# Kernel tuning notes

Hardware: AMD Instinct MI355X
Metric: run time of the kernel (lower is better)

## Reference

```python
import jax, jax.numpy as jnp
import numpy as np
import math

B, S, H = 2, 2048, 2048
NH, HD = 32, 64
BASE, SCALE = 10000.0, 2.0
MAX_POS, ORIG_MAX_POS = 8192, 8192
BETA_FAST, BETA_SLOW = 32, 1
EPS = 1e-6


def _yarn_cos_sin():
    # revised_yarn: scale inv_freq by 1/((1-mask)*scale + mask)
    inv_freq = 1.0 / BASE ** (np.arange(0, HD, 2, dtype=np.float64) / HD)
    def corr(nr):
        return HD * math.log(ORIG_MAX_POS / (nr * 2 * math.pi)) / (2 * math.log(BASE))
    low = max(math.floor(corr(BETA_FAST)), 0)
    high = min(math.ceil(corr(BETA_SLOW)), HD - 1)
    hi = high + 0.001 if low == high else high
    ramp = np.clip((np.arange(HD // 2, dtype=np.float64) - low) / (hi - low), 0.0, 1.0)
    mask = 1.0 - ramp  # extrapolation_factor = 1
    inv_freq = inv_freq / ((1.0 - mask) * SCALE + mask)
    mscale = (0.1 * math.log(SCALE) + 1.0) if SCALE > 1 else 1.0
    t = np.arange(MAX_POS, dtype=np.float64)
    freqs = np.outer(t, inv_freq)
    emb = np.concatenate([freqs, freqs], axis=-1)
    return np.cos(emb) * mscale, np.sin(emb) * mscale

_COS_NP, _SIN_NP = _yarn_cos_sin()


def rotate_half(x):
    x1, x2 = jnp.split(x, 2, axis=-1)
    return jnp.concatenate([-x2, x1], axis=-1)


def rms_norm(x, w):
    v = jnp.mean(jnp.square(x.astype(jnp.float32)), axis=-1, keepdims=True)
    return (x.astype(jnp.float32) * jax.lax.rsqrt(v + EPS)).astype(x.dtype) * w


def localized_filtering(x, lf1, lf2, w1, b1, w2, b2, ln_w):
    # x: (B,S,H); torch works in (B,H,S,1) with kernel-(2,1) convs over seq
    residual = x
    xi = jnp.transpose(x, (0, 2, 1))[:, :, :, None]  # (B,H,S,1)
    xi = jnp.concatenate([lf1, xi], axis=2)          # (B,H,S+1,1)
    dn = ('NCHW', 'OIHW', 'NCHW')
    o1 = jax.lax.conv_general_dilated(xi, w1, (1, 1), 'VALID', dimension_numbers=dn)
    o1 = o1 + b1[None, :, None, None]                # (B,H/2,S,1)
    o1c = jnp.concatenate([lf2, o1], axis=2)         # (B,H/2,S+1,1)
    o2 = jax.lax.conv_general_dilated(o1c, w2, (1, 1), 'VALID', dimension_numbers=dn)
    o2 = o2 + b2[None, :, None, None]                # (B,H,S,1)
    o2 = jnp.transpose(o2[:, :, :, 0], (0, 2, 1))    # (B,S,H)
    return rms_norm(o2 + residual, ln_w)


def setup_inputs():
    key = jax.random.key(0)
    ks = jax.random.split(key, 8)
    f = lambda k, shp: jax.random.normal(k, shp, dtype=jnp.float32) * 0.02
    return {
        'hidden_states': jax.random.normal(ks[0], (B, S, H), dtype=jnp.float32),
        'position_ids': jnp.broadcast_to(jnp.arange(S, dtype=jnp.int32)[None, :], (B, S)),
        'lf1_cache': jnp.zeros((B, H, 1, 1), jnp.float32),
        'lf2_cache': jnp.zeros((B, H // 2, 1, 1), jnp.float32),
        'Wqk': f(ks[1], (2 * H, H)),
        'Wv': f(ks[2], (H, H)),
        'Wo': f(ks[3], (H, H)),
        'conv1_w': f(ks[4], (H // 2, H, 2, 1)),
        'conv1_b': jnp.zeros((H // 2,), jnp.float32),
        'conv2_w': f(ks[5], (H, H // 2, 2, 1)),
        'conv2_b': jnp.zeros((H,), jnp.float32),
        'ln_w': jnp.ones((H,), jnp.float32),
    }


def reference(hidden_states, position_ids, lf1_cache, lf2_cache, Wqk, Wv, Wo,
              conv1_w, conv1_b, conv2_w, conv2_b, ln_w):
    cos = jnp.asarray(_COS_NP, jnp.float32)
    sin = jnp.asarray(_SIN_NP, jnp.float32)
    # v from raw hidden states
    v = (hidden_states @ Wv.T).reshape(B, S, NH, HD).transpose(0, 2, 1, 3)  # (B,NH,S,HD)
    # localized filtering gate feeds q/k projection
    lf = localized_filtering(hidden_states, lf1_cache, lf2_cache,
                             conv1_w, conv1_b, conv2_w, conv2_b, ln_w)
    qk = (lf @ Wqk.T).reshape(B, S, NH, 2 * HD)  # per-head [q|k] split
    q = qk[..., :HD].transpose(0, 2, 1, 3)       # (B,NH,S,HD)
    k = qk[..., HD:].transpose(0, 2, 1, 3)
    cos_p = cos[position_ids][:, None, :, :]     # (B,1,S,HD)
    sin_p = sin[position_ids][:, None, :, :]
    q = q * cos_p + rotate_half(q) * sin_p
    k = k * cos_p + rotate_half(k) * sin_p
    scores = jnp.einsum('bhqd,bhkd->bhqk', q, k) / math.sqrt(HD)
    causal = jnp.tril(jnp.ones((S, S), dtype=bool))
    scores = jnp.where(causal[None, None], scores, jnp.finfo(scores.dtype).min)
    attn = jax.nn.softmax(scores, axis=-1)
    ctx = jnp.einsum('bhqk,bhkd->bhqd', attn, v)
    out = ctx.transpose(0, 2, 1, 3).reshape(B, S, H) @ Wo.T
    return out
```

## Files before the change

kernel.cpp:

```cpp
#include <hip/hip_runtime.h>
#include <hip/hip_bf16.h>
#include <math.h>
#include <stdint.h>

typedef __hip_bfloat16 bf16;
using f32x4 = __attribute__((ext_vector_type(4))) float;
using s16x8 = __attribute__((ext_vector_type(8))) short;

constexpr int Bc = 2, Sc = 2048, Hc = 2048, NHc = 32, HDc = 64;
constexpr int Mc = Bc * Sc;
constexpr int MAXPOS = 8192;

constexpr size_t OFF_WV  = 0;
constexpr size_t OFF_WQK = OFF_WV  + (size_t)Hc * Hc * 2;
constexpr size_t OFF_WO  = OFF_WQK + (size_t)2 * Hc * Hc * 2;
constexpr size_t OFF_W1  = OFF_WO  + (size_t)Hc * Hc * 2;
constexpr size_t OFF_W2  = OFF_W1  + (size_t)(Hc/2) * (2*Hc) * 2;
constexpr size_t OFF_HS  = OFF_W2  + (size_t)Hc * Hc * 2;
constexpr size_t OFF_XPR = OFF_HS  + (size_t)Mc * Hc * 2;
constexpr size_t OFF_O1  = OFF_XPR + (size_t)Mc * Hc * 2;
constexpr size_t OFF_O1P = OFF_O1  + (size_t)Mc * (Hc/2) * 2;
constexpr size_t OFF_O2  = OFF_O1P + (size_t)Mc * (Hc/2) * 2;
constexpr size_t OFF_LF  = OFF_O2  + (size_t)Mc * Hc * 4;
constexpr size_t OFF_VT  = OFF_LF  + (size_t)Mc * Hc * 2;
constexpr size_t OFF_COS = OFF_VT  + (size_t)Mc * Hc * 2;
constexpr size_t OFF_SIN = OFF_COS + (size_t)MAXPOS * HDc * 4;
constexpr size_t OFF_QK  = OFF_O2;
constexpr size_t OFF_Q   = OFF_XPR;
constexpr size_t OFF_K   = OFF_HS;
constexpr size_t OFF_CTX = OFF_O1;

__device__ __forceinline__ f32x4 mfma16(s16x8 a, s16x8 b, f32x4 c) {
  return __builtin_amdgcn_mfma_f32_16x16x32_bf16(a, b, c, 0, 0, 0);
}
__device__ __forceinline__ void gload16(const bf16* g, bf16* l) {
  __builtin_amdgcn_global_load_lds(
      (__attribute__((address_space(1))) void*)g,
      (__attribute__((address_space(3))) void*)l, 16, 0, 0);
}
__device__ __forceinline__ uint16_t bfbits(float x) {
  union { bf16 h; uint16_t u; } v; v.h = __float2bfloat16(x); return v.u;
}
__device__ __forceinline__ uint32_t pkbf(float a, float b) {
  return (uint32_t)bfbits(a) | ((uint32_t)bfbits(b) << 16);
}

__global__ void k_cvt(const float* __restrict__ in, bf16* __restrict__ out, int n) {
  int i = blockIdx.x * 256 + threadIdx.x;
  if (i < n) out[i] = __float2bfloat16(in[i]);
}

__global__ void k_cvt_hs(const float* __restrict__ hs, const float* __restrict__ lf1,
                         bf16* __restrict__ hsb, bf16* __restrict__ xprev) {
  int i = blockIdx.x * 256 + threadIdx.x;
  if (i >= Mc * Hc) return;
  float v = hs[i];
  bf16 b = __float2bfloat16(v);
  hsb[i] = b;
  int row = i >> 11, col = i & (Hc - 1);
  int s = row & (Sc - 1), bb = row >> 11;
  if (s + 1 < Sc) xprev[i + Hc] = b;
  if (s == 0)     xprev[i] = __float2bfloat16(lf1[bb * Hc + col]);
}

__global__ void k_repack1(const float* __restrict__ w, bf16* __restrict__ out) {
  int i = blockIdx.x * 256 + threadIdx.x;
  if (i >= (Hc/2) * 2 * Hc) return;
  int oc = i >> 12, k = i & 4095;
  int ic = k & (Hc - 1), t = k >> 11;
  out[i] = __float2bfloat16(w[((size_t)oc * Hc + ic) * 2 + t]);
}
__global__ void k_repack2(const float* __restrict__ w, bf16* __restrict__ out) {
  int i = blockIdx.x * 256 + threadIdx.x;
  if (i >= Hc * Hc) return;
  int c = i >> 11, k = i & (Hc - 1);
  int oc = k & (Hc/2 - 1), t = k >> 10;
  out[i] = __float2bfloat16(w[((size_t)c * (Hc/2) + oc) * 2 + t]);
}

__global__ void k_prefill_o1p(const float* __restrict__ lf2, bf16* __restrict__ o1p) {
  int i = blockIdx.x * 256 + threadIdx.x;
  if (i >= Bc * (Hc/2)) return;
  int b = i >> 10, n = i & (Hc/2 - 1);
  o1p[(size_t)b * Sc * (Hc/2) + n] = __float2bfloat16(lf2[i]);
}

struct InvF { double v[32]; double mscale; };

__global__ void k_costab(InvF f, float* __restrict__ ct, float* __restrict__ st) {
  int i = blockIdx.x * 256 + threadIdx.x;
  if (i >= MAXPOS * HDc) return;
  int p = i >> 6, d = i & 63;
  double ang = (double)p * f.v[d & 31];
  ct[i] = (float)(cos(ang) * f.mscale);
  st[i] = (float)(sin(ang) * f.mscale);
}

__global__ __launch_bounds__(256) void k_rmsnorm(const float* __restrict__ x,
                                                 const float* __restrict__ w,
                                                 bf16* __restrict__ out) {
  __shared__ float red[4];
  int row = blockIdx.x;
  const float* xr = x + (size_t)row * Hc;
  float ss = 0.f;
  for (int c = threadIdx.x; c < Hc; c += 256) { float v = xr[c]; ss += v * v; }
  for (int off = 32; off; off >>= 1) ss += __shfl_down(ss, off, 64);
  if ((threadIdx.x & 63) == 0) red[threadIdx.x >> 6] = ss;
  __syncthreads();
  float sc = rsqrtf((red[0] + red[1] + red[2] + red[3]) / Hc + 1e-6f);
  for (int c = threadIdx.x; c < Hc; c += 256)
    out[(size_t)row * Hc + c] = __float2bfloat16(xr[c] * sc * w[c]);
}

__global__ void k_rope(const bf16* __restrict__ qk, const int* __restrict__ pos,
                       const float* __restrict__ ct, const float* __restrict__ st,
                       bf16* __restrict__ qo, bf16* __restrict__ ko) {
  const float QSC = 0.125f * 1.44269504088896f;
  int i = blockIdx.x * 256 + threadIdx.x;
  if (i >= Mc * NHc * 32) return;
  int d = i & 31, h = (i >> 5) & 31, row = i >> 10;
  int p = pos[row];
  float c0 = ct[p * 64 + d],      s0 = st[p * 64 + d];
  float c1 = ct[p * 64 + 32 + d], s1 = st[p * 64 + 32 + d];
  const bf16* base = qk + (size_t)row * 4096 + h * 128;
  float q0 = __bfloat162float(base[d]),      q1 = __bfloat162float(base[d + 32]);
  float k0 = __bfloat162float(base[64 + d]), k1 = __bfloat162float(base[96 + d]);
  int b = row >> 11, s = row & (Sc - 1);
  size_t o = ((size_t)(b * NHc + h) * Sc + s) * 64 + d;
  qo[o]      = __float2bfloat16((q0 * c0 - q1 * s0) * QSC);
  qo[o + 32] = __float2bfloat16((q1 * c1 + q0 * s1) * QSC);
  ko[o]      = __float2bfloat16(k0 * c0 - k1 * s0);
  ko[o + 32] = __float2bfloat16(k1 * c1 + k0 * s1);
}

template <int EPI, int BM = 128>
__global__ __launch_bounds__(256) void gemm_bt(
    const bf16* __restrict__ A0, const bf16* __restrict__ A1, int Ksplit,
    const bf16* __restrict__ Bw, int K, int N, void* __restrict__ Cout,
    const float* __restrict__ bias, const float* __restrict__ resid,
    bf16* __restrict__ aux) {
  constexpr int MR = BM / 32;
  __shared__ __align__(16) bf16 As[2][BM * 32];
  __shared__ __align__(16) bf16 Bs[2][128 * 32];
  const int tid = threadIdx.x;
  const int gx = gridDim.x;
  const int lin = blockIdx.y * gx + blockIdx.x;
  const int nwg = gx * gridDim.y;
  const int swz = (lin & 7) * (nwg >> 3) + (lin >> 3);
  const int bn = swz % gx, bm = swz / gx;
  const int w = tid >> 6, l = tid & 63;
  const int wm = (w >> 1) * (BM / 2), wn = (w & 1) * 64;
  const int lrow = l & 15, lg = l >> 4, lk = lg * 8;
  const int r0 = tid >> 2, cofs = (tid & 3) * 8;

  auto stage = [&](int buf, int kt) {
    const int kcol = kt * 32;
    const bf16* Au; int kc;
    if (kcol < Ksplit) { Au = A0; kc = kcol; } else { Au = A1; kc = kcol - Ksplit; }
    gload16(Au + (size_t)(bm * BM + r0) * Ksplit + kc + cofs,        &As[buf][tid * 8]);
    if constexpr (BM == 128)
      gload16(Au + (size_t)(bm * BM + r0 + 64) * Ksplit + kc + cofs, &As[buf][2048 + tid * 8]);
    gload16(Bw + (size_t)(bn * 128 + r0) * K + kcol + cofs,          &Bs[buf][tid * 8]);
    gload16(Bw + (size_t)(bn * 128 + r0 + 64) * K + kcol + cofs,     &Bs[buf][2048 + tid * 8]);
  };

  f32x4 acc[MR][4] = {};
  const int nkt = K / 32;
  stage(0, 0);
  __syncthreads();
  for (int kt = 0; kt < nkt; ++kt) {
    const int cur = kt & 1;
    if (kt + 1 < nkt) stage(cur ^ 1, kt + 1);
    s16x8 af[MR], bfr[4];
#pragma unroll
    for (int m = 0; m < MR; ++m)
      af[m] = *(const s16x8*)&As[cur][(wm + m * 16 + lrow) * 32 + lk];
#pragma unroll
    for (int n = 0; n < 4; ++n)
      bfr[n] = *(const s16x8*)&Bs[cur][(wn + n * 16 + lrow) * 32 + lk];
    __builtin_amdgcn_s_setprio(1);
#pragma unroll
    for (int m = 0; m < MR; ++m)
#pragma unroll
      for (int n = 0; n < 4; ++n)
        acc[m][n] = mfma16(af[m], bfr[n], acc[m][n]);
    __builtin_amdgcn_s_setprio(0);
    __syncthreads();
  }
#pragma unroll
  for (int m = 0; m < MR; ++m)
#pragma unroll
    for (int n = 0; n < 4; ++n)
#pragma unroll
      for (int r = 0; r < 4; ++r) {
        const int grow = bm * BM + wm + m * 16 + lg * 4 + r;
        const int gcol = bn * 128 + wn + n * 16 + lrow;
        float v = acc[m][n][r];
        if constexpr (EPI == 0) {
          ((bf16*)Cout)[(size_t)grow * N + gcol] = __float2bfloat16(v);
        } else if constexpr (EPI == 1) {
          v += bias[gcol];
          bf16 bv = __float2bfloat16(v);
          ((bf16*)Cout)[(size_t)grow * N + gcol] = bv;
          if ((grow & (Sc - 1)) != Sc - 1) aux[(size_t)(grow + 1) * N + gcol] = bv;
        } else if constexpr (EPI == 2) {
          v += bias[gcol] + resid[(size_t)grow * N + gcol];
          ((float*)Cout)[(size_t)grow * N + gcol] = v;
        } else if constexpr (EPI == 5) {
          const int b = gcol >> 11, s = gcol & (Sc - 1);
          ((bf16*)Cout)[((size_t)(b * Hc + grow)) * Sc + s] = __float2bfloat16(v);
        } else {
          ((float*)Cout)[(size_t)grow * N + gcol] = v;
        }
      }
}

__global__ __launch_bounds__(256) void k_attn(const bf16* __restrict__ Q,
                                              const bf16* __restrict__ Kg,
                                              const bf16* __restrict__ Vt,
                                              bf16* __restrict__ ctx) {
  __shared__ __align__(16) bf16 Ks[2][64 * 64];
  __shared__ __align__(16) bf16 Vs[2][64 * 64];
  __shared__ __align__(16) uint32_t Pl[4][2][2][16][20];
  const int tid = threadIdx.x;
  const int w = tid >> 6, l = tid & 63;
  const int lrow = l & 15, lg = l >> 4, lk = lg * 8;
  const int bh = blockIdx.x;
  const int tile = blockIdx.y;
  const bf16* Qp = Q  + (size_t)bh * Sc * HDc;
  const bf16* Kp = Kg + (size_t)bh * Sc * HDc;
  const bf16* Vp = Vt + (size_t)bh * HDc * Sc;
  const int b = bh >> 5, h = bh & 31;
  const s16x8 ones8 = {16256, 16256, 16256, 16256, 16256, 16256, 16256, 16256};

  const int srow0 = tid >> 3, schunk = tid & 7;

  for (int pass = 0; pass < 2; ++pass) {
    const int base = (pass == 0) ? tile * 128 : (Sc - 128 - tile * 128);
    const int q0 = base + w * 32;
    const int NT = base / 64 + 2;

    s16x8 qa[2][2];
#pragma unroll
    for (int m = 0; m < 2; ++m)
#pragma unroll
      for (int hf = 0; hf < 2; ++hf)
        qa[m][hf] = *(const s16x8*)&Qp[(size_t)(q0 + m * 16 + lrow) * 64 + hf * 32 + lk];

    f32x4 o[2][4] = {};
    f32x4 lsf[2] = {};
    float mx[2] = {-1e30f, -1e30f};

    {
      const int kv0 = 0;
      gload16(Kp + (size_t)(kv0 + srow0) * 64 + ((schunk ^ (srow0 & 7)) << 3),
              &Ks[0][tid * 8]);
      gload16(Kp + (size_t)(kv0 + 32 + srow0) * 64 + ((schunk ^ ((32 + srow0) & 7)) << 3),
              &Ks[0][2048 + tid * 8]);
      gload16(Vp + (size_t)srow0 * Sc + kv0 + ((schunk ^ (srow0 & 7)) << 3),
              &Vs[0][tid * 8]);
      gload16(Vp + (size_t)(32 + srow0) * Sc + kv0 + ((schunk ^ ((32 + srow0) & 7)) << 3),
              &Vs[0][2048 + tid * 8]);
    }
    __syncthreads();

    for (int t = 0; t < NT; ++t) {
      const int cur = t & 1;
      const int kv0 = t * 64;
      if (t + 1 < NT) {
        const int nkv = kv0 + 64;
        const int nb = cur ^ 1;
        gload16(Kp + (size_t)(nkv + srow0) * 64 + ((schunk ^ (srow0 & 7)) << 3),
                &Ks[nb][tid * 8]);
        gload16(Kp + (size_t)(nkv + 32 + srow0) * 64 + ((schunk ^ ((32 + srow0) & 7)) << 3),
                &Ks[nb][2048 + tid * 8]);
        gload16(Vp + (size_t)srow0 * Sc + nkv + ((schunk ^ (srow0 & 7)) << 3),
                &Vs[nb][tid * 8]);
        gload16(Vp + (size_t)(32 + srow0) * Sc + nkv + ((schunk ^ ((32 + srow0) & 7)) << 3),
                &Vs[nb][2048 + tid * 8]);
      }
      if (kv0 <= q0) {
        s16x8 kc[8], vc[4][2];
#pragma unroll
        for (int c = 0; c < 4; ++c)
#pragma unroll
          for (int hf = 0; hf < 2; ++hf) {
            const int row = c * 16 + lrow;
            kc[c * 2 + hf] =
                *(const s16x8*)&Ks[cur][row * 64 + (((hf << 2) + lg) ^ (row & 7)) * 8];
          }
#pragma unroll
        for (int db = 0; db < 4; ++db)
#pragma unroll
          for (int kh = 0; kh < 2; ++kh) {
            const int row = db * 16 + lrow;
            vc[db][kh] =
                *(const s16x8*)&Vs[cur][row * 64 + (((kh << 2) + lg) ^ (row & 7)) * 8];
          }
        const bool lastit = (kv0 + 64 > q0);

#pragma unroll
        for (int m = 0; m < 2; ++m) {
          f32x4 s[4];
          __builtin_amdgcn_s_setprio(1);
#pragma unroll
          for (int c = 0; c < 4; ++c) {
            f32x4 z = {};
            z = mfma16(kc[c * 2], qa[m][0], z);
            z = mfma16(kc[c * 2 + 1], qa[m][1], z);
            s[c] = z;
          }
          __builtin_amdgcn_s_setprio(0);

          if (lastit) {
            const int qq = q0 + m * 16 + lrow;
#pragma unroll
            for (int c = 0; c < 4; ++c)
#pragma unroll
              for (int r = 0; r < 4; ++r)
                if (kv0 + c * 16 + lg * 4 + r > qq) s[c][r] = -1e30f;
          }
          float t16 = fmaxf(
              fmaxf(fmaxf(fmaxf(s[0][0], s[0][1]), fmaxf(s[0][2], s[0][3])),
                    fmaxf(fmaxf(s[1][0], s[1][1]), fmaxf(s[1][2], s[1][3]))),
              fmaxf(fmaxf(fmaxf(s[2][0], s[2][1]), fmaxf(s[2][2], s[2][3])),
                    fmaxf(fmaxf(s[3][0], s[3][1]), fmaxf(s[3][2], s[3][3]))));
          if (!__all(t16 <= mx[m] + 8.0f)) {
            t16 = fmaxf(t16, __shfl_xor(t16, 16, 64));
            t16 = fmaxf(t16, __shfl_xor(t16, 32, 64));
            const float mnew = fmaxf(mx[m], t16);
            const float sold = __builtin_amdgcn_exp2f(mx[m] - mnew);
            mx[m] = mnew;
            lsf[m] *= sold;
#pragma unroll
            for (int db = 0; db < 4; ++db) o[m][db] *= sold;
          }
          float p[4][4];
#pragma unroll
          for (int c = 0; c < 4; ++c)
#pragma unroll
            for (int r = 0; r < 4; ++r)
              p[c][r] = __builtin_amdgcn_exp2f(s[c][r] - mx[m]);
#pragma unroll
          for (int kh = 0; kh < 2; ++kh) {
            *(uint64_t*)&Pl[w][m][kh][lrow][lg * 2] =
                (uint64_t)pkbf(p[kh * 2][0], p[kh * 2][1]) |
                ((uint64_t)pkbf(p[kh * 2][2], p[kh * 2][3]) << 32);
            *(uint64_t*)&Pl[w][m][kh][lrow][8 + lg * 2] =
                (uint64_t)pkbf(p[kh * 2 + 1][0], p[kh * 2 + 1][1]) |
                ((uint64_t)pkbf(p[kh * 2 + 1][2], p[kh * 2 + 1][3]) << 32);
          }
          const s16x8 pb0 = *(const s16x8*)&Pl[w][m][0][lrow][lg * 4];
          const s16x8 pb1 = *(const s16x8*)&Pl[w][m][1][lrow][lg * 4];
          __builtin_amdgcn_s_setprio(1);
#pragma unroll
          for (int db = 0; db < 4; ++db) o[m][db] = mfma16(vc[db][0], pb0, o[m][db]);
          lsf[m] = mfma16(ones8, pb0, lsf[m]);
#pragma unroll
          for (int db = 0; db < 4; ++db) o[m][db] = mfma16(vc[db][1], pb1, o[m][db]);
          lsf[m] = mfma16(ones8, pb1, lsf[m]);
          __builtin_amdgcn_s_setprio(0);
        }
      }
      __syncthreads();
    }
#pragma unroll
    for (int m = 0; m < 2; ++m) {
      const float inv = 1.0f / lsf[m][0];
      const int qrow = q0 + m * 16 + lrow;
      const size_t rowoff = ((size_t)(b * Sc + qrow)) * Hc + h * 64;
#pragma unroll
      for (int db = 0; db < 4; ++db) {
        uint64_t pk = (uint64_t)bfbits(o[m][db][0] * inv) |
                      ((uint64_t)bfbits(o[m][db][1] * inv) << 16) |
                      ((uint64_t)bfbits(o[m][db][2] * inv) << 32) |
                      ((uint64_t)bfbits(o[m][db][3] * inv) << 48);
        *(uint64_t*)&ctx[rowoff + db * 16 + lg * 4] = pk;
      }
    }
    __syncthreads();
  }
}

extern "C" void kernel_launch(void* const* d_in, const int* in_sizes, int n_in,
                              void* d_out, int out_size, void* d_ws, size_t ws_size,
                              hipStream_t stream) {
  (void)in_sizes; (void)n_in; (void)out_size; (void)ws_size;
  const float* hs  = (const float*)d_in[0];
  const int*   pos = (const int*)d_in[1];
  const float* lf1 = (const float*)d_in[2];
  const float* lf2 = (const float*)d_in[3];
  const float* Wqk = (const float*)d_in[4];
  const float* Wv  = (const float*)d_in[5];
  const float* Wo  = (const float*)d_in[6];
  const float* c1w = (const float*)d_in[7];
  const float* c1b = (const float*)d_in[8];
  const float* c2w = (const float*)d_in[9];
  const float* c2b = (const float*)d_in[10];
  const float* lnw = (const float*)d_in[11];
  float* out = (float*)d_out;
  char*  ws  = (char*)d_ws;

  bf16* wvB   = (bf16*)(ws + OFF_WV);
  bf16* wqkB  = (bf16*)(ws + OFF_WQK);
  bf16* woB   = (bf16*)(ws + OFF_WO);
  bf16* w1B   = (bf16*)(ws + OFF_W1);
  bf16* w2B   = (bf16*)(ws + OFF_W2);
  bf16* hsB   = (bf16*)(ws + OFF_HS);
  bf16* xprB  = (bf16*)(ws + OFF_XPR);
  bf16* o1B   = (bf16*)(ws + OFF_O1);
  bf16* o1pB  = (bf16*)(ws + OFF_O1P);
  float* o2F  = (float*)(ws + OFF_O2);
  bf16* lfB   = (bf16*)(ws + OFF_LF);
  bf16* vtB   = (bf16*)(ws + OFF_VT);
  float* cosT = (float*)(ws + OFF_COS);
  float* sinT = (float*)(ws + OFF_SIN);
  bf16* qkB   = (bf16*)(ws + OFF_QK);
  bf16* qB    = (bf16*)(ws + OFF_Q);
  bf16* kB    = (bf16*)(ws + OFF_K);
  bf16* ctxB  = (bf16*)(ws + OFF_CTX);

  InvF f;
  {
    const double base = 10000.0, scale = 2.0;
    const int hd = HDc;
    auto corr = [&](double nr) {
      return hd * log(8192.0 / (nr * 2.0 * M_PI)) / (2.0 * log(base));
    };
    double low = floor(corr(32.0)); if (low < 0) low = 0;
    double high = ceil(corr(1.0));  if (high > hd - 1) high = hd - 1;
    double hi = (low == high) ? high + 0.001 : high;
    for (int i = 0; i < 32; ++i) {
      double inv = 1.0 / pow(base, (2.0 * i) / hd);
      double ramp = ((double)i - low) / (hi - low);
      ramp = ramp < 0.0 ? 0.0 : (ramp > 1.0 ? 1.0 : ramp);
      double mask = 1.0 - ramp;
      f.v[i] = inv / ((1.0 - mask) * scale + mask);
    }
    f.mscale = 0.1 * log(scale) + 1.0;
  }

  k_cvt<<<(Hc * Hc + 255) / 256, 256, 0, stream>>>(Wv, wvB, Hc * Hc);
  k_cvt<<<(2 * Hc * Hc + 255) / 256, 256, 0, stream>>>(Wqk, wqkB, 2 * Hc * Hc);
  k_cvt<<<(Hc * Hc + 255) / 256, 256, 0, stream>>>(Wo, woB, Hc * Hc);
  k_repack1<<<((Hc / 2) * 2 * Hc + 255) / 256, 256, 0, stream>>>(c1w, w1B);
  k_repack2<<<(Hc * Hc + 255) / 256, 256, 0, stream>>>(c2w, w2B);
  k_cvt_hs<<<(Mc * Hc + 255) / 256, 256, 0, stream>>>(hs, lf1, hsB, xprB);
  k_prefill_o1p<<<(Bc * (Hc / 2) + 255) / 256, 256, 0, stream>>>(lf2, o1pB);
  k_costab<<<(MAXPOS * HDc + 255) / 256, 256, 0, stream>>>(f, cosT, sinT);

  gemm_bt<1, 64><<<dim3((Hc / 2) / 128, Mc / 64), 256, 0, stream>>>(
      xprB, hsB, Hc, w1B, 2 * Hc, Hc / 2, o1B, c1b, nullptr, o1pB);
  gemm_bt<5><<<dim3(Mc / 128, Hc / 128), 256, 0, stream>>>(
      wvB, wvB, Hc, hsB, Hc, Mc, vtB, nullptr, nullptr, nullptr);
  gemm_bt<2><<<dim3(Hc / 128, Mc / 128), 256, 0, stream>>>(
      o1pB, o1B, Hc / 2, w2B, Hc, Hc, o2F, c2b, hs, nullptr);
  k_rmsnorm<<<Mc, 256, 0, stream>>>(o2F, lnw, lfB);
  gemm_bt<0><<<dim3((2 * Hc) / 128, Mc / 128), 256, 0, stream>>>(
      lfB, lfB, Hc, wqkB, Hc, 2 * Hc, qkB, nullptr, nullptr, nullptr);
  k_rope<<<(Mc * NHc * 32 + 255) / 256, 256, 0, stream>>>(qkB, pos, cosT, sinT, qB, kB);
  k_attn<<<dim3(64, 8), 256, 0, stream>>>(qB, kB, vtB, ctxB);
  gemm_bt<4><<<dim3(Hc / 128, Mc / 128), 256, 0, stream>>>(
      ctxB, ctxB, Hc, woB, Hc, Hc, out, nullptr, nullptr, nullptr);
}
```

Before: 505.1 us.

## Add 512-thread 256-row GEMM with triple-buffered LDS pipeline for big projections

Adds a new gemm8 kernel that uses 8 waves, 256-row tiles (256x128 or 256x256), a three-stage LDS ring with explicit vmcnt waits, an XOR-swizzled LDS layout and a chunked XCD-aware block remap. The V, conv2, QK and output projections are switched to it, while the conv1 GEMM keeps the old kernel with its swizzle removed. The aim is more data reuse per tile and better overlap of global loads with MFMA work, at the cost of more registers and LDS per block and lower occupancy.

```diff
diff --git a/kernel.cpp b/kernel.cpp
--- a/kernel.cpp
+++ b/kernel.cpp
@@ -44,6 +44,18 @@
 __device__ __forceinline__ uint32_t pkbf(float a, float b) {
   return (uint32_t)bfbits(a) | ((uint32_t)bfbits(b) << 16);
 }
+__device__ __forceinline__ void block_bar() {
+  asm volatile("" ::: "memory");
+  __builtin_amdgcn_s_barrier();
+  asm volatile("" ::: "memory");
+}
+template <int N> __device__ __forceinline__ void vm_wait() {
+  if constexpr (N == 0)      asm volatile("s_waitcnt vmcnt(0)" ::: "memory");
+  else if constexpr (N == 3) asm volatile("s_waitcnt vmcnt(3)" ::: "memory");
+  else if constexpr (N == 4) asm volatile("s_waitcnt vmcnt(4)" ::: "memory");
+  else if constexpr (N == 6) asm volatile("s_waitcnt vmcnt(6)" ::: "memory");
+  else if constexpr (N == 8) asm volatile("s_waitcnt vmcnt(8)" ::: "memory");
+}
 
 __global__ void k_cvt(const float* __restrict__ in, bf16* __restrict__ out, int n) {
   int i = blockIdx.x * 256 + threadIdx.x;
@@ -143,11 +155,7 @@
   __shared__ __align__(16) bf16 As[2][BM * 32];
   __shared__ __align__(16) bf16 Bs[2][128 * 32];
   const int tid = threadIdx.x;
-  const int gx = gridDim.x;
-  const int lin = blockIdx.y * gx + blockIdx.x;
-  const int nwg = gx * gridDim.y;
-  const int swz = (lin & 7) * (nwg >> 3) + (lin >> 3);
-  const int bn = swz % gx, bm = swz / gx;
+  const int bm = blockIdx.y, bn = blockIdx.x;
   const int w = tid >> 6, l = tid & 63;
   const int wm = (w >> 1) * (BM / 2), wn = (w & 1) * 64;
   const int lrow = l & 15, lg = l >> 4, lk = lg * 8;
@@ -196,13 +204,98 @@
         const int grow = bm * BM + wm + m * 16 + lg * 4 + r;
         const int gcol = bn * 128 + wn + n * 16 + lrow;
         float v = acc[m][n][r];
-        if constexpr (EPI == 0) {
-          ((bf16*)Cout)[(size_t)grow * N + gcol] = __float2bfloat16(v);
-        } else if constexpr (EPI == 1) {
+        if constexpr (EPI == 1) {
           v += bias[gcol];
           bf16 bv = __float2bfloat16(v);
           ((bf16*)Cout)[(size_t)grow * N + gcol] = bv;
           if ((grow & (Sc - 1)) != Sc - 1) aux[(size_t)(grow + 1) * N + gcol] = bv;
+        } else {
+          ((float*)Cout)[(size_t)grow * N + gcol] = v;
+        }
+      }
+}
+
+template <int EPI, int BN>
+__global__ __launch_bounds__(512, 2) void gemm8(
+    const bf16* __restrict__ A0, const bf16* __restrict__ A1, int Ksplit,
+    const bf16* __restrict__ Bw, int K, int N, void* __restrict__ Cout,
+    const float* __restrict__ bias, const float* __restrict__ resid) {
+  constexpr int BM = 256;
+  constexpr int L = (BN == 256) ? 4 : 3;
+  constexpr int TILE = (BM + BN) * 32;
+  constexpr int MR = (BN == 256) ? 8 : 4;
+  __shared__ __align__(16) bf16 lds[3][TILE];
+  const int tid = threadIdx.x;
+  const int w = tid >> 6, l = tid & 63;
+  const int lrow = l & 15, lg = l >> 4;
+  const int wm = (BN == 256) ? (w >> 2) * 128 : (w & 3) * 64;
+  const int wn = (BN == 256) ? (w & 3) * 64 : (w >> 2) * 64;
+  const int gx = gridDim.x;
+  const int lin = blockIdx.y * gx + blockIdx.x;
+  const int cx = gx >> 2, cy = gridDim.y >> 1;
+  const int c = lin & 7, idx = lin >> 3;
+  const int bn = (c & 3) * cx + idx % cx;
+  const int bm = (c >> 2) * cy + idx / cx;
+
+  auto ld1 = [&](const bf16* srcbase, size_t stride, bf16* ldst, int ci) {
+    const int pr = ci >> 3, rem = ci & 7;
+    const int r = pr * 2 + (rem >> 2), g = (rem & 3) ^ (pr & 3);
+    gload16(srcbase + (size_t)r * stride + g * 8, ldst + ci * 8);
+  };
+  auto stage = [&](int kt, int slot) {
+    const int kcol = kt * 32;
+    const bf16* Au; int kc;
+    if (kcol < Ksplit) { Au = A0; kc = kcol; } else { Au = A1; kc = kcol - Ksplit; }
+    const bf16* As_ = Au + (size_t)bm * BM * Ksplit + kc;
+    bf16* ldsA = lds[slot];
+    ld1(As_, Ksplit, ldsA, tid);
+    ld1(As_, Ksplit, ldsA, tid + 512);
+    const bf16* Bs_ = Bw + (size_t)bn * BN * K + kcol;
+    bf16* ldsB = lds[slot] + BM * 32;
+    ld1(Bs_, K, ldsB, tid);
+    if constexpr (BN == 256) ld1(Bs_, K, ldsB, tid + 512);
+  };
+  auto frag = [&](const bf16* base, int r) -> s16x8 {
+    const int s = ((r >> 1) << 3) + ((r & 1) << 2) + (lg ^ ((r >> 1) & 3));
+    return *(const s16x8*)(base + s * 8);
+  };
+
+  f32x4 acc[MR][4] = {};
+  const int nkt = K / 32;
+  stage(0, 0);
+  stage(1, 1);
+  for (int t = 0; t < nkt; ++t) {
+    if (t + 2 < nkt) { stage(t + 2, (t + 2) % 3); vm_wait<2 * L>(); }
+    else if (t + 1 < nkt) { vm_wait<L>(); }
+    else { vm_wait<0>(); }
+    block_bar();
+    const bf16* Asl = lds[t % 3];
+    const bf16* Bsl = Asl + BM * 32;
+    s16x8 af[MR], bfr[4];
+#pragma unroll
+    for (int m = 0; m < MR; ++m) af[m] = frag(Asl, wm + m * 16 + lrow);
+#pragma unroll
+    for (int n = 0; n < 4; ++n) bfr[n] = frag(Bsl, wn + n * 16 + lrow);
+    __builtin_amdgcn_s_setprio(1);
+#pragma unroll
+    for (int m = 0; m < MR; ++m)
+#pragma unroll
+      for (int n = 0; n < 4; ++n)
+        acc[m][n] = mfma16(af[m], bfr[n], acc[m][n]);
+    __builtin_amdgcn_s_setprio(0);
+    block_bar();
+  }
+#pragma unroll
+  for (int m = 0; m < MR; ++m)
+#pragma unroll
+    for (int n = 0; n < 4; ++n)
+#pragma unroll
+      for (int r = 0; r < 4; ++r) {
+        const int grow = bm * BM + wm + m * 16 + lg * 4 + r;
+        const int gcol = bn * BN + wn + n * 16 + lrow;
+        float v = acc[m][n][r];
+        if constexpr (EPI == 0) {
+          ((bf16*)Cout)[(size_t)grow * N + gcol] = __float2bfloat16(v);
         } else if constexpr (EPI == 2) {
           v += bias[gcol] + resid[(size_t)grow * N + gcol];
           ((float*)Cout)[(size_t)grow * N + gcol] = v;
@@ -252,14 +345,11 @@
     float mx[2] = {-1e30f, -1e30f};
 
     {
-      const int kv0 = 0;
-      gload16(Kp + (size_t)(kv0 + srow0) * 64 + ((schunk ^ (srow0 & 7)) << 3),
-              &Ks[0][tid * 8]);
-      gload16(Kp + (size_t)(kv0 + 32 + srow0) * 64 + ((schunk ^ ((32 + srow0) & 7)) << 3),
+      gload16(Kp + (size_t)srow0 * 64 + ((schunk ^ (srow0 & 7)) << 3), &Ks[0][tid * 8]);
+      gload16(Kp + (size_t)(32 + srow0) * 64 + ((schunk ^ ((32 + srow0) & 7)) << 3),
               &Ks[0][2048 + tid * 8]);
-      gload16(Vp + (size_t)srow0 * Sc + kv0 + ((schunk ^ (srow0 & 7)) << 3),
-              &Vs[0][tid * 8]);
-      gload16(Vp + (size_t)(32 + srow0) * Sc + kv0 + ((schunk ^ ((32 + srow0) & 7)) << 3),
+      gload16(Vp + (size_t)srow0 * Sc + ((schunk ^ (srow0 & 7)) << 3), &Vs[0][tid * 8]);
+      gload16(Vp + (size_t)(32 + srow0) * Sc + ((schunk ^ ((32 + srow0) & 7)) << 3),
               &Vs[0][2048 + tid * 8]);
     }
     __syncthreads();
@@ -451,15 +541,15 @@
 
   gemm_bt<1, 64><<<dim3((Hc / 2) / 128, Mc / 64), 256, 0, stream>>>(
       xprB, hsB, Hc, w1B, 2 * Hc, Hc / 2, o1B, c1b, nullptr, o1pB);
-  gemm_bt<5><<<dim3(Mc / 128, Hc / 128), 256, 0, stream>>>(
-      wvB, wvB, Hc, hsB, Hc, Mc, vtB, nullptr, nullptr, nullptr);
-  gemm_bt<2><<<dim3(Hc / 128, Mc / 128), 256, 0, stream>>>(
-      o1pB, o1B, Hc / 2, w2B, Hc, Hc, o2F, c2b, hs, nullptr);
+  gemm8<5, 128><<<dim3(Mc / 128, Hc / 256), 512, 0, stream>>>(
+      wvB, wvB, Hc, hsB, Hc, Mc, vtB, nullptr, nullptr);
+  gemm8<2, 128><<<dim3(Hc / 128, Mc / 256), 512, 0, stream>>>(
+      o1pB, o1B, Hc / 2, w2B, Hc, Hc, o2F, c2b, hs);
   k_rmsnorm<<<Mc, 256, 0, stream>>>(o2F, lnw, lfB);
-  gemm_bt<0><<<dim3((2 * Hc) / 128, Mc / 128), 256, 0, stream>>>(
-      lfB, lfB, Hc, wqkB, Hc, 2 * Hc, qkB, nullptr, nullptr, nullptr);
+  gemm8<0, 256><<<dim3((2 * Hc) / 256, Mc / 256), 512, 0, stream>>>(
+      lfB, lfB, Hc, wqkB, Hc, 2 * Hc, qkB, nullptr, nullptr);
   k_rope<<<(Mc * NHc * 32 + 255) / 256, 256, 0, stream>>>(qkB, pos, cosT, sinT, qB, kB);
   k_attn<<<dim3(64, 8), 256, 0, stream>>>(qB, kB, vtB, ctxB);
-  gemm_bt<4><<<dim3(Hc / 128, Mc / 128), 256, 0, stream>>>(
-      ctxB, ctxB, Hc, woB, Hc, Hc, out, nullptr, nullptr, nullptr);
-}
+  gemm8<4, 128><<<dim3(Hc / 128, Mc / 256), 512, 0, stream>>>(
+      ctxB, ctxB, Hc, woB, Hc, Hc, out, nullptr, nullptr);
+}
```

New measurement: 472.9 us. 6.4% less time.
